# Optimization experiments

Hardware: AMD Instinct MI355X
Metric: run time of the kernel (lower is better)

## Reference

```python
import jax, jax.numpy as jnp
import numpy as np

N_NODES = 100000
N_EDGES = 1600000
RBF_DIM = 64
DIM = 64


def shifted_softplus(x):
    # torch.nn.Softplus(beta=0.5, threshold=14): (1/0.5)*log(1+exp(0.5*x)),
    # with linear passthrough when 0.5*x > 14.
    half = 0.5 * x
    return jnp.where(half > 14.0, x, 2.0 * jnp.logaddexp(0.0, half))


def setup_inputs() -> dict:
    key = jax.random.key(0)
    ks = jax.random.split(key, 8)
    node_weight = jax.random.normal(ks[0], (N_NODES, DIM), dtype=jnp.float32)
    rbf_out = jax.random.normal(ks[1], (N_EDGES, RBF_DIM), dtype=jnp.float32)
    # Linear params (torch Linear: y = x @ W.T + b); store W already transposed as (in,out)
    s1 = 1.0 / np.sqrt(RBF_DIM)
    s2 = 1.0 / np.sqrt(DIM)
    W1 = jax.random.uniform(ks[2], (RBF_DIM, DIM), jnp.float32, -s1, s1)
    b1 = jax.random.uniform(ks[3], (DIM,), jnp.float32, -s1, s1)
    W2 = jax.random.uniform(ks[4], (DIM, DIM), jnp.float32, -s2, s2)
    b2 = jax.random.uniform(ks[5], (DIM,), jnp.float32, -s2, s2)
    src = jax.random.randint(ks[6], (N_EDGES,), 0, N_NODES, dtype=jnp.int32)
    dst = jax.random.randint(ks[7], (N_EDGES,), 0, N_NODES, dtype=jnp.int32)
    return {
        "node_weight": node_weight, "rbf_out": rbf_out,
        "W1": W1, "b1": b1, "W2": W2, "b2": b2,
        "src": src, "dst": dst, "n_nodes": N_NODES,
    }


def reference(node_weight, rbf_out, W1, b1, W2, b2, src, dst, n_nodes):
    # edge MLP: Linear -> shifted softplus -> Linear, on rbf features  [E, dim]
    e = shifted_softplus(rbf_out @ W1 + b1) @ W2 + b2
    # gather source node weight per edge, multiply by edge filter      [E, dim]
    m = node_weight[src] * e
    # scatter-sum messages into destination nodes                      [N, dim]
    h = jax.ops.segment_sum(m, dst, num_segments=n_nodes)
    return h
```

## Files before the change

### kernel.cpp

```cpp
#include <hip/hip_runtime.h>
#include <math.h>

typedef short bf16x8 __attribute__((ext_vector_type(8)));
typedef float f32x4 __attribute__((ext_vector_type(4)));

__device__ __forceinline__ short f2bf(float f) {
    union { float f; unsigned u; } v; v.f = f;
    unsigned r = v.u + 0x7fffu + ((v.u >> 16) & 1u);
    return (short)(r >> 16);
}

__device__ __forceinline__ float ssp(float x) {
    float h = 0.5f * x;
    return 2.0f * (fmaxf(h, 0.0f) + __logf(1.0f + __expf(-fabsf(h))));
}

__global__ void hist_kernel(const int* __restrict__ dst, int* __restrict__ counts,
                            int n_edges) {
    int i = blockIdx.x * blockDim.x + threadIdx.x;
    int gs = gridDim.x * blockDim.x;
    for (int e = i; e < n_edges; e += gs) atomicAdd(&counts[dst[e]], 1);
}

__global__ __launch_bounds__(256) void scan_blocks(const int* __restrict__ counts,
        int* __restrict__ base, int* __restrict__ partials, int n) {
    __shared__ int wsum[4];
    const int tid = threadIdx.x, lane = tid & 63, wv = tid >> 6;
    const int i0 = blockIdx.x * 1024 + tid * 4;
    int c[4], ts = 0;
    #pragma unroll
    for (int j = 0; j < 4; ++j) { c[j] = (i0 + j < n) ? counts[i0 + j] : 0; ts += c[j]; }
    int x = ts;
    #pragma unroll
    for (int off = 1; off < 64; off <<= 1) {
        int y = __shfl_up(x, off);
        if (lane >= off) x += y;
    }
    if (lane == 63) wsum[wv] = x;
    __syncthreads();
    int woff = 0;
    for (int w = 0; w < wv; ++w) woff += wsum[w];
    int run = woff + x - ts;
    #pragma unroll
    for (int j = 0; j < 4; ++j) { if (i0 + j < n) base[i0 + j] = run; run += c[j]; }
    if (tid == 255) partials[blockIdx.x] = woff + x;
}

__global__ void scan_partials(int* __restrict__ partials, int nblk) {
    const int lane = threadIdx.x;
    int carry = 0;
    for (int b = 0; b < nblk; b += 64) {
        const int i = b + lane;
        int v = (i < nblk) ? partials[i] : 0;
        int x = v;
        #pragma unroll
        for (int off = 1; off < 64; off <<= 1) {
            int y = __shfl_up(x, off);
            if (lane >= off) x += y;
        }
        if (i < nblk) partials[i] = carry + x - v;
        carry += __shfl(x, 63);
    }
}

__global__ __launch_bounds__(256) void add_offsets(int* __restrict__ base,
        const int* __restrict__ partials, int n, int total) {
    const int i0 = blockIdx.x * 1024 + threadIdx.x * 4;
    const int p = partials[blockIdx.x];
    #pragma unroll
    for (int j = 0; j < 4; ++j) if (i0 + j < n) base[i0 + j] += p;
    if (blockIdx.x == 0 && threadIdx.x == 0) base[n] = total;
}

__global__ void scatter_kernel(const int* __restrict__ dst, const int* __restrict__ src,
        const int* __restrict__ base, int* __restrict__ cursor,
        int* __restrict__ perm, int* __restrict__ sp, int* __restrict__ dp,
        int n_edges) {
    int i = blockIdx.x * blockDim.x + threadIdx.x;
    int gs = gridDim.x * blockDim.x;
    for (int e = i; e < n_edges; e += gs) {
        int d = dst[e];
        int off = atomicAdd(&cursor[d], 1);
        int pos = base[d] + off;
        perm[pos] = e;
        sp[pos] = src[e];
        dp[pos] = d;
    }
}

__global__ __launch_bounds__(256, 2) void cfconv_perm(
    const float* __restrict__ nw, const float* __restrict__ rbf,
    const float* __restrict__ W1, const float* __restrict__ b1,
    const float* __restrict__ W2, const float* __restrict__ b2,
    const int* __restrict__ perm, const int* __restrict__ sp,
    const int* __restrict__ dp,
    float* __restrict__ out, int n_edges)
{
    __shared__ __align__(16) short lds_h[4][16 * 72];

    const int tid  = threadIdx.x;
    const int wave = tid >> 6;
    const int lane = tid & 63;
    const int l16  = lane & 15;
    const int quad = lane >> 4;

    bf16x8 w1f[2][4], w2f[2][4];
    #pragma unroll
    for (int ks = 0; ks < 2; ++ks) {
        #pragma unroll
        for (int nt = 0; nt < 4; ++nt) {
            const int col = l16 + 16 * nt;
            const int k0  = quad * 8 + 32 * ks;
            bf16x8 a, b;
            #pragma unroll
            for (int j = 0; j < 8; ++j) {
                a[j] = f2bf(W1[(k0 + j) * 64 + col]);
                b[j] = f2bf(W2[(k0 + j) * 64 + col]);
            }
            w1f[ks][nt] = a;
            w2f[ks][nt] = b;
        }
    }
    float b1v[4], b2v[4];
    #pragma unroll
    for (int nt = 0; nt < 4; ++nt) {
        b1v[nt] = b1[l16 + 16 * nt];
        b2v[nt] = b2[l16 + 16 * nt];
    }

    short* myh = lds_h[wave];
    const int ntiles = (n_edges + 15) >> 4;
    const int gw = blockIdx.x * 4 + wave;
    const int stride = gridDim.x * 4;

    for (int t = gw; t < ntiles; t += stride) {
        const int p0 = t * 16;

        int prow = p0 + l16;
        if (prow >= n_edges) prow = n_edges - 1;
        const int e_a = perm[prow];
        const float* rp = rbf + (size_t)e_a * 64 + quad * 8;
        bf16x8 af[2];
        #pragma unroll
        for (int ks = 0; ks < 2; ++ks) {
            float4 lo = *(const float4*)(rp + 32 * ks);
            float4 hi = *(const float4*)(rp + 32 * ks + 4);
            bf16x8 a;
            a[0] = f2bf(lo.x); a[1] = f2bf(lo.y); a[2] = f2bf(lo.z); a[3] = f2bf(lo.w);
            a[4] = f2bf(hi.x); a[5] = f2bf(hi.y); a[6] = f2bf(hi.z); a[7] = f2bf(hi.w);
            af[ks] = a;
        }

        f32x4 acc[4] = { {0.f,0.f,0.f,0.f}, {0.f,0.f,0.f,0.f},
                         {0.f,0.f,0.f,0.f}, {0.f,0.f,0.f,0.f} };
        #pragma unroll
        for (int nt = 0; nt < 4; ++nt)
            #pragma unroll
            for (int ks = 0; ks < 2; ++ks)
                acc[nt] = __builtin_amdgcn_mfma_f32_16x16x32_bf16(
                    af[ks], w1f[ks][nt], acc[nt], 0, 0, 0);

        #pragma unroll
        for (int nt = 0; nt < 4; ++nt)
            #pragma unroll
            for (int r = 0; r < 4; ++r)
                myh[(quad * 4 + r) * 72 + l16 + 16 * nt] =
                    f2bf(ssp(acc[nt][r] + b1v[nt]));

        bf16x8 hf[2];
        #pragma unroll
        for (int ks = 0; ks < 2; ++ks)
            hf[ks] = *(const bf16x8*)(myh + l16 * 72 + quad * 8 + 32 * ks);

        f32x4 acc2[4] = { {0.f,0.f,0.f,0.f}, {0.f,0.f,0.f,0.f},
                          {0.f,0.f,0.f,0.f}, {0.f,0.f,0.f,0.f} };
        #pragma unroll
        for (int nt = 0; nt < 4; ++nt)
            #pragma unroll
            for (int ks = 0; ks < 2; ++ks)
                acc2[nt] = __builtin_amdgcn_mfma_f32_16x16x32_bf16(
                    hf[ks], w2f[ks][nt], acc2[nt], 0, 0, 0);

        int   dr[4];
        float msg[4][4];
        #pragma unroll
        for (int r = 0; r < 4; ++r) {
            const int row = p0 + quad * 4 + r;
            if (row < n_edges) {
                const int s = sp[row];
                dr[r] = dp[row];
                const float* nwp = nw + (size_t)s * 64;
                #pragma unroll
                for (int nt = 0; nt < 4; ++nt)
                    msg[r][nt] = (acc2[nt][r] + b2v[nt]) * nwp[l16 + 16 * nt];
            } else {
                dr[r] = 0x7fffffff;
                #pragma unroll
                for (int nt = 0; nt < 4; ++nt) msg[r][nt] = 0.f;
            }
        }

        int cur = __shfl(dr[0], l16);
        while (true) {
            float s0 = 0.f, s1 = 0.f, s2 = 0.f, s3 = 0.f;
            #pragma unroll
            for (int r = 0; r < 4; ++r) {
                if (dr[r] == cur) {
                    s0 += msg[r][0]; s1 += msg[r][1];
                    s2 += msg[r][2]; s3 += msg[r][3];
                }
            }
            s0 += __shfl_xor(s0, 16); s0 += __shfl_xor(s0, 32);
            s1 += __shfl_xor(s1, 16); s1 += __shfl_xor(s1, 32);
            s2 += __shfl_xor(s2, 16); s2 += __shfl_xor(s2, 32);
            s3 += __shfl_xor(s3, 16); s3 += __shfl_xor(s3, 32);
            float o = s0;
            o = (quad == 1) ? s1 : o;
            o = (quad == 2) ? s2 : o;
            o = (quad == 3) ? s3 : o;
            atomicAdd(out + (size_t)cur * 64 + quad * 16 + l16, o);

            int nxt = 0x7fffffff;
            #pragma unroll
            for (int r = 0; r < 4; ++r)
                if (dr[r] > cur && dr[r] < nxt) nxt = dr[r];
            int tmp = __shfl_xor(nxt, 16); nxt = (tmp < nxt) ? tmp : nxt;
            tmp = __shfl_xor(nxt, 32);     nxt = (tmp < nxt) ? tmp : nxt;
            if (nxt == 0x7fffffff) break;
            cur = nxt;
        }
    }
}

__global__ __launch_bounds__(256, 2) void cfconv_kernel(
    const float* __restrict__ nw, const float* __restrict__ rbf,
    const float* __restrict__ W1, const float* __restrict__ b1,
    const float* __restrict__ W2, const float* __restrict__ b2,
    const int* __restrict__ src, const int* __restrict__ dst,
    float* __restrict__ out, int n_edges)
{
    __shared__ __align__(16) short lds_h[4][16 * 72];

    const int tid  = threadIdx.x;
    const int wave = tid >> 6;
    const int lane = tid & 63;
    const int l16  = lane & 15;
    const int quad = lane >> 4;

    bf16x8 w1f[2][4], w2f[2][4];
    #pragma unroll
    for (int ks = 0; ks < 2; ++ks) {
        #pragma unroll
        for (int nt = 0; nt < 4; ++nt) {
            const int col = l16 + 16 * nt;
            const int k0  = quad * 8 + 32 * ks;
            bf16x8 a, b;
            #pragma unroll
            for (int j = 0; j < 8; ++j) {
                a[j] = f2bf(W1[(k0 + j) * 64 + col]);
                b[j] = f2bf(W2[(k0 + j) * 64 + col]);
            }
            w1f[ks][nt] = a;
            w2f[ks][nt] = b;
        }
    }
    float b1v[4], b2v[4];
    #pragma unroll
    for (int nt = 0; nt < 4; ++nt) {
        b1v[nt] = b1[l16 + 16 * nt];
        b2v[nt] = b2[l16 + 16 * nt];
    }

    short* myh = lds_h[wave];
    const int ntiles = (n_edges + 15) >> 4;
    const int gw = blockIdx.x * 4 + wave;
    const int stride = gridDim.x * 4;

    for (int t = gw; t < ntiles; t += stride) {
        const int e0 = t * 16;
        int arow = e0 + l16;
        if (arow >= n_edges) arow = n_edges - 1;
        const float* rp = rbf + (size_t)arow * 64 + quad * 8;
        bf16x8 af[2];
        #pragma unroll
        for (int ks = 0; ks < 2; ++ks) {
            float4 lo = *(const float4*)(rp + 32 * ks);
            float4 hi = *(const float4*)(rp + 32 * ks + 4);
            bf16x8 a;
            a[0] = f2bf(lo.x); a[1] = f2bf(lo.y); a[2] = f2bf(lo.z); a[3] = f2bf(lo.w);
            a[4] = f2bf(hi.x); a[5] = f2bf(hi.y); a[6] = f2bf(hi.z); a[7] = f2bf(hi.w);
            af[ks] = a;
        }

        f32x4 acc[4] = { {0.f,0.f,0.f,0.f}, {0.f,0.f,0.f,0.f},
                         {0.f,0.f,0.f,0.f}, {0.f,0.f,0.f,0.f} };
        #pragma unroll
        for (int nt = 0; nt < 4; ++nt)
            #pragma unroll
            for (int ks = 0; ks < 2; ++ks)
                acc[nt] = __builtin_amdgcn_mfma_f32_16x16x32_bf16(
                    af[ks], w1f[ks][nt], acc[nt], 0, 0, 0);

        #pragma unroll
        for (int nt = 0; nt < 4; ++nt)
            #pragma unroll
            for (int r = 0; r < 4; ++r)
                myh[(quad * 4 + r) * 72 + l16 + 16 * nt] =
                    f2bf(ssp(acc[nt][r] + b1v[nt]));

        bf16x8 hf[2];
        #pragma unroll
        for (int ks = 0; ks < 2; ++ks)
            hf[ks] = *(const bf16x8*)(myh + l16 * 72 + quad * 8 + 32 * ks);

        f32x4 acc2[4] = { {0.f,0.f,0.f,0.f}, {0.f,0.f,0.f,0.f},
                          {0.f,0.f,0.f,0.f}, {0.f,0.f,0.f,0.f} };
        #pragma unroll
        for (int nt = 0; nt < 4; ++nt)
            #pragma unroll
            for (int ks = 0; ks < 2; ++ks)
                acc2[nt] = __builtin_amdgcn_mfma_f32_16x16x32_bf16(
                    hf[ks], w2f[ks][nt], acc2[nt], 0, 0, 0);

        #pragma unroll
        for (int r = 0; r < 4; ++r) {
            const int e = e0 + quad * 4 + r;
            if (e < n_edges) {
                const int s = src[e], d = dst[e];
                const float* nwp = nw + (size_t)s * 64;
                float* op = out + (size_t)d * 64;
                #pragma unroll
                for (int nt = 0; nt < 4; ++nt) {
                    const int col = l16 + 16 * nt;
                    atomicAdd(op + col, (acc2[nt][r] + b2v[nt]) * nwp[col]);
                }
            }
        }
    }
}

extern "C" void kernel_launch(void* const* d_in, const int* in_sizes, int n_in,
                              void* d_out, int out_size, void* d_ws, size_t ws_size,
                              hipStream_t stream) {
    const float* nw  = (const float*)d_in[0];
    const float* rbf = (const float*)d_in[1];
    const float* W1  = (const float*)d_in[2];
    const float* b1  = (const float*)d_in[3];
    const float* W2  = (const float*)d_in[4];
    const float* b2  = (const float*)d_in[5];
    const int*   src = (const int*)d_in[6];
    const int*   dst = (const int*)d_in[7];
    float* out = (float*)d_out;
    const int n_edges = in_sizes[6];
    const int n_nodes = out_size / 64;

    const size_t need = ((size_t)(n_nodes + 1) + (size_t)n_nodes + 1024
                         + 3 * (size_t)n_edges) * sizeof(int);

    if (ws_size >= need) {
        int* base     = (int*)d_ws;
        int* counts   = base + (n_nodes + 1);
        int* partials = counts + n_nodes;
        int* perm     = partials + 1024;
        int* sp       = perm + n_edges;
        int* dp       = sp + n_edges;

        const int nblk = (n_nodes + 1023) / 1024;
        int eblocks = (n_edges + 255) / 256;
        if (eblocks > 8192) eblocks = 8192;

        hipMemsetAsync(counts, 0, (size_t)n_nodes * sizeof(int), stream);
        hipLaunchKernelGGL(hist_kernel, dim3(eblocks), dim3(256), 0, stream,
                           dst, counts, n_edges);
        hipLaunchKernelGGL(scan_blocks, dim3(nblk), dim3(256), 0, stream,
                           counts, base, partials, n_nodes);
        hipLaunchKernelGGL(scan_partials, dim3(1), dim3(64), 0, stream,
                           partials, nblk);
        hipLaunchKernelGGL(add_offsets, dim3(nblk), dim3(256), 0, stream,
                           base, partials, n_nodes, n_edges);
        hipMemsetAsync(counts, 0, (size_t)n_nodes * sizeof(int), stream);
        hipLaunchKernelGGL(scatter_kernel, dim3(eblocks), dim3(256), 0, stream,
                           dst, src, base, counts, perm, sp, dp, n_edges);

        hipMemsetAsync(out, 0, (size_t)out_size * sizeof(float), stream);
        hipLaunchKernelGGL(cfconv_perm, dim3(1024), dim3(256), 0, stream,
                           nw, rbf, W1, b1, W2, b2, perm, sp, dp, out, n_edges);
    } else {
        hipMemsetAsync(out, 0, (size_t)out_size * sizeof(float), stream);
        hipLaunchKernelGGL(cfconv_kernel, dim3(1024), dim3(256), 0, stream,
                           nw, rbf, W1, b1, W2, b2, src, dst, out, n_edges);
    }
}
```

Baseline: 883.8 us.

## Software-pipeline edge index and rbf loads; init scatter cursor from offsets

The edge-tile loop in cfconv_perm is restructured to prefetch the next tile's perm, src and dst indices and its rbf rows while the current tile's MFMAs and atomics run. Node-weight gathers are issued before the first matmul, and src/dst are loaded as int4 vectors. add_offsets now writes a separate cursor array holding absolute positions, which removes one memset and the base lookup in the scatter kernel. Launch bounds are raised to 4 blocks per SM, which caps registers per thread even though the prefetch buffers add register pressure, so spills are possible.

```diff
diff --git a/kernel.cpp b/kernel.cpp
--- a/kernel.cpp
+++ b/kernel.cpp
@@ -64,31 +64,47 @@
 }
 
 __global__ __launch_bounds__(256) void add_offsets(int* __restrict__ base,
-        const int* __restrict__ partials, int n, int total) {
+        const int* __restrict__ partials, int* __restrict__ cursor,
+        int n, int total) {
     const int i0 = blockIdx.x * 1024 + threadIdx.x * 4;
     const int p = partials[blockIdx.x];
     #pragma unroll
-    for (int j = 0; j < 4; ++j) if (i0 + j < n) base[i0 + j] += p;
+    for (int j = 0; j < 4; ++j)
+        if (i0 + j < n) {
+            int v = base[i0 + j] + p;
+            base[i0 + j] = v;
+            cursor[i0 + j] = v;
+        }
     if (blockIdx.x == 0 && threadIdx.x == 0) base[n] = total;
 }
 
 __global__ void scatter_kernel(const int* __restrict__ dst, const int* __restrict__ src,
-        const int* __restrict__ base, int* __restrict__ cursor,
+        int* __restrict__ cursor,
         int* __restrict__ perm, int* __restrict__ sp, int* __restrict__ dp,
         int n_edges) {
     int i = blockIdx.x * blockDim.x + threadIdx.x;
     int gs = gridDim.x * blockDim.x;
     for (int e = i; e < n_edges; e += gs) {
         int d = dst[e];
-        int off = atomicAdd(&cursor[d], 1);
-        int pos = base[d] + off;
+        int pos = atomicAdd(&cursor[d], 1);
         perm[pos] = e;
         sp[pos] = src[e];
         dp[pos] = d;
     }
 }
 
-__global__ __launch_bounds__(256, 2) void cfconv_perm(
+__device__ __forceinline__ int4 load_idx4(const int* __restrict__ p, int b, int n) {
+    if (b + 3 < n) return *(const int4*)(p + b);
+    int4 v;
+    int c0 = b     < n ? b     : n - 1;
+    int c1 = b + 1 < n ? b + 1 : n - 1;
+    int c2 = b + 2 < n ? b + 2 : n - 1;
+    int c3 = b + 3 < n ? b + 3 : n - 1;
+    v.x = p[c0]; v.y = p[c1]; v.z = p[c2]; v.w = p[c3];
+    return v;
+}
+
+__global__ __launch_bounds__(256, 4) void cfconv_perm(
     const float* __restrict__ nw, const float* __restrict__ rbf,
     const float* __restrict__ W1, const float* __restrict__ b1,
     const float* __restrict__ W2, const float* __restrict__ b2,
@@ -133,24 +149,59 @@
     const int gw = blockIdx.x * 4 + wave;
     const int stride = gridDim.x * 4;
 
-    for (int t = gw; t < ntiles; t += stride) {
+    int t = gw;
+    if (t >= ntiles) return;
+
+    int ea; int4 spq, dpq;
+    float4 ra, rb, rc, rd;
+    {
         const int p0 = t * 16;
-
         int prow = p0 + l16;
         if (prow >= n_edges) prow = n_edges - 1;
-        const int e_a = perm[prow];
-        const float* rp = rbf + (size_t)e_a * 64 + quad * 8;
+        ea  = perm[prow];
+        spq = load_idx4(sp, p0 + quad * 4, n_edges);
+        dpq = load_idx4(dp, p0 + quad * 4, n_edges);
+        const float* rp = rbf + (size_t)ea * 64 + quad * 8;
+        ra = *(const float4*)(rp);
+        rb = *(const float4*)(rp + 4);
+        rc = *(const float4*)(rp + 32);
+        rd = *(const float4*)(rp + 36);
+    }
+
+    for (; t < ntiles; ) {
+        const int p0 = t * 16;
+        const int tn = t + stride;
+
+        int ea_n = 0; int4 spq_n, dpq_n;
+        if (tn < ntiles) {
+            const int p0n = tn * 16;
+            int prow = p0n + l16;
+            if (prow >= n_edges) prow = n_edges - 1;
+            ea_n  = perm[prow];
+            spq_n = load_idx4(sp, p0n + quad * 4, n_edges);
+            dpq_n = load_idx4(dp, p0n + quad * 4, n_edges);
+        }
+
+        const int sarr[4] = { spq.x, spq.y, spq.z, spq.w };
+        float nwv[4][4];
+        #pragma unroll
+        for (int r = 0; r < 4; ++r) {
+            const float* nwp = nw + (size_t)sarr[r] * 64;
+            #pragma unroll
+            for (int nt = 0; nt < 4; ++nt)
+                nwv[r][nt] = nwp[l16 + 16 * nt];
+        }
+
         bf16x8 af[2];
-        #pragma unroll
-        for (int ks = 0; ks < 2; ++ks) {
-            float4 lo = *(const float4*)(rp + 32 * ks);
-            float4 hi = *(const float4*)(rp + 32 * ks + 4);
+        {
             bf16x8 a;
-            a[0] = f2bf(lo.x); a[1] = f2bf(lo.y); a[2] = f2bf(lo.z); a[3] = f2bf(lo.w);
-            a[4] = f2bf(hi.x); a[5] = f2bf(hi.y); a[6] = f2bf(hi.z); a[7] = f2bf(hi.w);
-            af[ks] = a;
-        }
-
+            a[0] = f2bf(ra.x); a[1] = f2bf(ra.y); a[2] = f2bf(ra.z); a[3] = f2bf(ra.w);
+            a[4] = f2bf(rb.x); a[5] = f2bf(rb.y); a[6] = f2bf(rb.z); a[7] = f2bf(rb.w);
+            af[0] = a;
+            a[0] = f2bf(rc.x); a[1] = f2bf(rc.y); a[2] = f2bf(rc.z); a[3] = f2bf(rc.w);
+            a[4] = f2bf(rd.x); a[5] = f2bf(rd.y); a[6] = f2bf(rd.z); a[7] = f2bf(rd.w);
+            af[1] = a;
+        }
         f32x4 acc[4] = { {0.f,0.f,0.f,0.f}, {0.f,0.f,0.f,0.f},
                          {0.f,0.f,0.f,0.f}, {0.f,0.f,0.f,0.f} };
         #pragma unroll
@@ -181,23 +232,23 @@
                 acc2[nt] = __builtin_amdgcn_mfma_f32_16x16x32_bf16(
                     hf[ks], w2f[ks][nt], acc2[nt], 0, 0, 0);
 
-        int   dr[4];
-        float msg[4][4];
+        float4 ra_n, rb_n, rc_n, rd_n;
+        if (tn < ntiles) {
+            const float* rp = rbf + (size_t)ea_n * 64 + quad * 8;
+            ra_n = *(const float4*)(rp);
+            rb_n = *(const float4*)(rp + 4);
+            rc_n = *(const float4*)(rp + 32);
+            rd_n = *(const float4*)(rp + 36);
+        }
+
+        const int darr[4] = { dpq.x, dpq.y, dpq.z, dpq.w };
+        int dr[4];
         #pragma unroll
         for (int r = 0; r < 4; ++r) {
-            const int row = p0 + quad * 4 + r;
-            if (row < n_edges) {
-                const int s = sp[row];
-                dr[r] = dp[row];
-                const float* nwp = nw + (size_t)s * 64;
-                #pragma unroll
-                for (int nt = 0; nt < 4; ++nt)
-                    msg[r][nt] = (acc2[nt][r] + b2v[nt]) * nwp[l16 + 16 * nt];
-            } else {
-                dr[r] = 0x7fffffff;
-                #pragma unroll
-                for (int nt = 0; nt < 4; ++nt) msg[r][nt] = 0.f;
-            }
+            dr[r] = (p0 + quad * 4 + r < n_edges) ? darr[r] : 0x7fffffff;
+            #pragma unroll
+            for (int nt = 0; nt < 4; ++nt)
+                acc2[nt][r] = (acc2[nt][r] + b2v[nt]) * nwv[r][nt];
         }
 
         int cur = __shfl(dr[0], l16);
@@ -206,8 +257,8 @@
             #pragma unroll
             for (int r = 0; r < 4; ++r) {
                 if (dr[r] == cur) {
-                    s0 += msg[r][0]; s1 += msg[r][1];
-                    s2 += msg[r][2]; s3 += msg[r][3];
+                    s0 += acc2[0][r]; s1 += acc2[1][r];
+                    s2 += acc2[2][r]; s3 += acc2[3][r];
                 }
             }
             s0 += __shfl_xor(s0, 16); s0 += __shfl_xor(s0, 32);
@@ -229,6 +280,10 @@
             if (nxt == 0x7fffffff) break;
             cur = nxt;
         }
+
+        t = tn;
+        ea = ea_n; spq = spq_n; dpq = dpq_n;
+        ra = ra_n; rb = rb_n; rc = rc_n; rd = rd_n;
     }
 }
 
@@ -354,17 +409,22 @@
     const int n_edges = in_sizes[6];
     const int n_nodes = out_size / 64;
 
-    const size_t need = ((size_t)(n_nodes + 1) + (size_t)n_nodes + 1024
-                         + 3 * (size_t)n_edges) * sizeof(int);
+    size_t off = 0;
+    auto carve = [&](size_t cnt) {
+        int* p = (int*)d_ws + off;
+        off += (cnt + 3) & ~(size_t)3;
+        return p;
+    };
+    int* base     = carve((size_t)n_nodes + 1);
+    int* counts   = carve(n_nodes);
+    int* partials = carve(1024);
+    int* cursor   = carve(n_nodes);
+    int* perm     = carve(n_edges);
+    int* sp       = carve(n_edges);
+    int* dp       = carve(n_edges);
+    const size_t need = off * sizeof(int);
 
     if (ws_size >= need) {
-        int* base     = (int*)d_ws;
-        int* counts   = base + (n_nodes + 1);
-        int* partials = counts + n_nodes;
-        int* perm     = partials + 1024;
-        int* sp       = perm + n_edges;
-        int* dp       = sp + n_edges;
-
         const int nblk = (n_nodes + 1023) / 1024;
         int eblocks = (n_edges + 255) / 256;
         if (eblocks > 8192) eblocks = 8192;
@@ -377,10 +437,9 @@
         hipLaunchKernelGGL(scan_partials, dim3(1), dim3(64), 0, stream,
                            partials, nblk);
         hipLaunchKernelGGL(add_offsets, dim3(nblk), dim3(256), 0, stream,
-                           base, partials, n_nodes, n_edges);
-        hipMemsetAsync(counts, 0, (size_t)n_nodes * sizeof(int), stream);
+                           base, partials, cursor, n_nodes, n_edges);
         hipLaunchKernelGGL(scatter_kernel, dim3(eblocks), dim3(256), 0, stream,
-                           dst, src, base, counts, perm, sp, dp, n_edges);
+                           dst, src, cursor, perm, sp, dp, n_edges);
 
         hipMemsetAsync(out, 0, (size_t)out_size * sizeof(float), stream);
         hipLaunchKernelGGL(cfconv_perm, dim3(1024), dim3(256), 0, stream,
```

Measured after the change: 919.0 us. 4.0% more time.
